# Performance work log

Measured on AMD Instinct MI355X. Metric: run time of the kernel, lower is better.

The kernel has to match this reference:

```python
import jax, jax.numpy as jnp
import numpy as np

N_NODES = 50000
N_EDGES = 1600000
FEAT = 1536
HID = 200
NCLS = 2


def setup_inputs() -> dict:
    key = jax.random.key(0)
    ks = jax.random.split(key, 12)
    x = jax.random.normal(ks[0], (N_NODES, FEAT), dtype=jnp.float32)
    edge_src = jax.random.randint(ks[1], (N_EDGES,), 0, N_NODES, dtype=jnp.int32)
    edge_dst = jax.random.randint(ks[2], (N_EDGES,), 0, N_NODES, dtype=jnp.int32)
    edge_w = jax.random.uniform(ks[3], (N_EDGES,), dtype=jnp.float32)
    s1 = 1.0 / np.sqrt(768.0)
    s2 = 1.0 / np.sqrt(HID)
    return {
        "x": x,
        "edge_src": edge_src,
        "edge_dst": edge_dst,
        "edge_w": edge_w,
        "W1a": jax.random.normal(ks[4], (768, HID), dtype=jnp.float32) * s1,
        "b1a": jnp.zeros((HID,), jnp.float32),
        "W2a": jax.random.normal(ks[5], (HID, NCLS), dtype=jnp.float32) * s2,
        "b2a": jnp.zeros((NCLS,), jnp.float32),
        "W1b": jax.random.normal(ks[6], (768, HID), dtype=jnp.float32) * s1,
        "b1b": jnp.zeros((HID,), jnp.float32),
        "W2b": jax.random.normal(ks[7], (HID, NCLS), dtype=jnp.float32) * s2,
        "b2b": jnp.zeros((NCLS,), jnp.float32),
    }


def _gcn_conv(x, W, b, src, dst, w, activation):
    # GCNConv: activation(A @ (X @ W) + b) with sparse A given as edge list
    h = x @ W                                  # [N, out] dense transform first (out < in)
    msg = h[src] * w[:, None]                  # [E, out] weighted messages
    agg = jax.ops.segment_sum(msg, dst, num_segments=x.shape[0])  # [N, out]
    return activation(agg + b)


def reference(x, edge_src, edge_dst, edge_w, W1a, b1a, W2a, b2a, W1b, b1b, W2b, b2b):
    x1 = x[:, :768]
    x2 = x[:, 768:]
    # Expert 1 branch (dropout is identity at inference)
    h1 = _gcn_conv(x1, W1a, b1a, edge_src, edge_dst, edge_w, jax.nn.relu)
    p1 = _gcn_conv(h1, W2a, b2a, edge_src, edge_dst, edge_w,
                   lambda z: jax.nn.softmax(z, axis=-1))
    # Expert 2 branch
    h2 = _gcn_conv(x2, W1b, b1b, edge_src, edge_dst, edge_w, jax.nn.relu)
    p2 = _gcn_conv(h2, W2b, b2b, edge_src, edge_dst, edge_w,
                   lambda z: jax.nn.softmax(z, axis=-1))
    # Inference-mode soft voting: elementwise max then renormalize
    votes = jnp.maximum(p1, p2)
    votes = votes / jnp.sum(votes, axis=1, keepdims=True)
    return votes
```

## Files before the change

### kernel.cpp

```cpp
#include <hip/hip_runtime.h>
#include <hip/hip_fp16.h>

#define N_NODES 50000
#define N_EDGES 1600000
#define FEAT    1536
#define HID     200
#define HIDP    208
#define HID2    416
#define KDIM    768
#define NSTRIPE 16
#define STRW    3200
#define NKEYS   (N_NODES * NSTRIPE)
#define L0B     3125
#define L1B     13

typedef _Float16 half8 __attribute__((ext_vector_type(8)));
typedef _Float16 half4 __attribute__((ext_vector_type(4)));
typedef float   float4v __attribute__((ext_vector_type(4)));

__global__ void prep_kernel(const float* __restrict__ W1a, const float* __restrict__ b1a,
                            const float* __restrict__ W2a,
                            const float* __restrict__ W1b, const float* __restrict__ b1b,
                            const float* __restrict__ W2b,
                            _Float16* __restrict__ Wht, float* __restrict__ b1comb,
                            float* __restrict__ W2comb) {
  int i = blockIdx.x * 256 + threadIdx.x;
  if (i < 2 * HIDP * KDIM) {
    int br = i / (HIDP * KDIM);
    int r  = i % (HIDP * KDIM);
    int n = r / KDIM, k = r % KDIM;
    const float* W = br ? W1b : W1a;
    Wht[i] = (n < HID) ? (_Float16)W[k * HID + n] : (_Float16)0.0f;
  }
  if (i < HID2) {
    int br = i / HIDP, c = i % HIDP;
    const float* b  = br ? b1b : b1a;
    const float* W2 = br ? W2b : W2a;
    bool ok = (c < HID);
    b1comb[i]       = ok ? b[c]        : 0.0f;
    W2comb[2*i + 0] = ok ? W2[c*2 + 0] : 0.0f;
    W2comb[2*i + 1] = ok ? W2[c*2 + 1] : 0.0f;
  }
}

__global__ void hist_kernel(const int* __restrict__ src, const int* __restrict__ dst,
                            int* __restrict__ cnt) {
  int i = blockIdx.x * 256 + threadIdx.x;
  if (i < N_EDGES) {
    int key = dst[i] * NSTRIPE + src[i] / STRW;
    atomicAdd(&cnt[key], 1);
  }
}

__global__ void scanA_kernel(const int* __restrict__ cnt, int* __restrict__ bsum) {
  __shared__ int s[256];
  int t = threadIdx.x;
  s[t] = cnt[blockIdx.x * 256 + t];
  __syncthreads();
  for (int off = 128; off; off >>= 1) {
    if (t < off) s[t] += s[t + off];
    __syncthreads();
  }
  if (t == 0) bsum[blockIdx.x] = s[0];
}
__global__ void scanM1_kernel(const int* __restrict__ bsum, int* __restrict__ bsumB) {
  __shared__ int s[256];
  int t = threadIdx.x, i = blockIdx.x * 256 + t;
  s[t] = (i < L0B) ? bsum[i] : 0;
  __syncthreads();
  for (int off = 128; off; off >>= 1) {
    if (t < off) s[t] += s[t + off];
    __syncthreads();
  }
  if (t == 0) bsumB[blockIdx.x] = s[0];
}
__global__ void scanTop_kernel(const int* __restrict__ bsumB, int* __restrict__ boff2,
                               int* __restrict__ bptr) {
  if (threadIdx.x == 0) {
    int run = 0;
    for (int j = 0; j < L1B; ++j) { boff2[j] = run; run += bsumB[j]; }
    bptr[NKEYS] = run;
  }
}
__global__ void scanMid_kernel(const int* __restrict__ bsum, const int* __restrict__ boff2,
                               int* __restrict__ boff1) {
  __shared__ int s[256];
  int t = threadIdx.x, i = blockIdx.x * 256 + t;
  int v = (i < L0B) ? bsum[i] : 0;
  s[t] = v;
  __syncthreads();
  for (int off = 1; off < 256; off <<= 1) {
    int a = (t >= off) ? s[t - off] : 0;
    __syncthreads();
    s[t] += a;
    __syncthreads();
  }
  if (i < L0B) boff1[i] = boff2[blockIdx.x] + s[t] - v;
}
__global__ void scanLow_kernel(const int* __restrict__ cnt, const int* __restrict__ boff1,
                               int* __restrict__ bptr) {
  __shared__ int s[256];
  int t = threadIdx.x, i = blockIdx.x * 256 + t;
  int v = cnt[i];
  s[t] = v;
  __syncthreads();
  for (int off = 1; off < 256; off <<= 1) {
    int a = (t >= off) ? s[t - off] : 0;
    __syncthreads();
    s[t] += a;
    __syncthreads();
  }
  bptr[i] = boff1[blockIdx.x] + s[t] - v;
}

__global__ void permute_kernel(const int* __restrict__ src, const int* __restrict__ dst,
                               const float* __restrict__ w, const int* __restrict__ bptr,
                               int* __restrict__ cnt2, int2* __restrict__ ssw) {
  int i = blockIdx.x * 256 + threadIdx.x;
  if (i < N_EDGES) {
    int key = dst[i] * NSTRIPE + src[i] / STRW;
    int pos = bptr[key] + atomicAdd(&cnt2[key], 1);
    ssw[pos] = make_int2(src[i], __float_as_int(w[i]));
  }
}

__global__ __launch_bounds__(256, 2) void gemm1_kernel(const float* __restrict__ x,
    const _Float16* __restrict__ Wht, _Float16* __restrict__ hpre) {
  const int m0 = blockIdx.x * 128;
  const int br = blockIdx.y;
  const int tid = threadIdx.x;
  const int wave = tid >> 6, lane = tid & 63;
  __shared__ _Float16 Alds[128][40];
  __shared__ _Float16 Blds[HIDP][40];
  const _Float16* Wb = Wht + (size_t)br * HIDP * KDIM;
  float4v acc[2][13];
#pragma unroll
  for (int mt = 0; mt < 2; ++mt)
#pragma unroll
    for (int nt = 0; nt < 13; ++nt) acc[mt][nt] = (float4v){0.f, 0.f, 0.f, 0.f};

  const int mlo = lane & 15, kq = (lane >> 4) * 8;

  for (int k0 = 0; k0 < KDIM; k0 += 32) {
    __syncthreads();
#pragma unroll
    for (int p = 0; p < 4; ++p) {
      int idx = tid + p * 256;
      int row = idx >> 3, c4 = idx & 7;
      int grow = m0 + row; if (grow > N_NODES - 1) grow = N_NODES - 1;
      const float4v xv = *(const float4v*)(x + (size_t)grow * FEAT + br * KDIM + k0 + c4 * 4);
      half4 hv = {(_Float16)xv[0], (_Float16)xv[1], (_Float16)xv[2], (_Float16)xv[3]};
      *(half4*)&Alds[row][c4 * 4] = hv;
    }
    for (int idx = tid; idx < HIDP * 4; idx += 256) {
      int n = idx >> 2, c = idx & 3;
      *(half8*)&Blds[n][c * 8] = *(const half8*)(Wb + n * KDIM + k0 + c * 8);
    }
    __syncthreads();
    half8 a0 = *(half8*)&Alds[wave * 32 + mlo][kq];
    half8 a1 = *(half8*)&Alds[wave * 32 + 16 + mlo][kq];
#pragma unroll
    for (int nt = 0; nt < 13; ++nt) {
      half8 b = *(half8*)&Blds[nt * 16 + mlo][kq];
      acc[0][nt] = __builtin_amdgcn_mfma_f32_16x16x32_f16(a0, b, acc[0][nt], 0, 0, 0);
      acc[1][nt] = __builtin_amdgcn_mfma_f32_16x16x32_f16(a1, b, acc[1][nt], 0, 0, 0);
    }
  }
  const int nlo = lane & 15, mq = (lane >> 4) * 4;
#pragma unroll
  for (int mt = 0; mt < 2; ++mt)
#pragma unroll
    for (int nt = 0; nt < 13; ++nt)
#pragma unroll
      for (int r = 0; r < 4; ++r) {
        int row = m0 + wave * 32 + mt * 16 + mq + r;
        if (row < N_NODES)
          hpre[(size_t)row * HID2 + br * HIDP + nt * 16 + nlo] = (_Float16)acc[mt][nt][r];
      }
}

__global__ __launch_bounds__(64) void agg1_kernel(const int2* __restrict__ ssw,
    const int* __restrict__ bptr, const _Float16* __restrict__ hpre,
    const float* __restrict__ b1comb, const float* __restrict__ W2comb,
    float4v* __restrict__ qtab) {
  const int d = blockIdx.x;
  const int lane = threadIdx.x;
  const int e0 = bptr[d * NSTRIPE], e1 = bptr[d * NSTRIPE + NSTRIPE];
  float acc[8];
#pragma unroll
  for (int j = 0; j < 8; ++j) acc[j] = 0.f;
  if (lane < 52) {
    const _Float16* hp = hpre + lane * 8;
    int e = e0;
    for (; e + 3 < e1; e += 4) {
      int2 s0 = ssw[e], s1 = ssw[e + 1], s2 = ssw[e + 2], s3 = ssw[e + 3];
      half8 h0 = *(const half8*)(hp + (size_t)s0.x * HID2);
      half8 h1 = *(const half8*)(hp + (size_t)s1.x * HID2);
      half8 h2 = *(const half8*)(hp + (size_t)s2.x * HID2);
      half8 h3 = *(const half8*)(hp + (size_t)s3.x * HID2);
      float w0 = __int_as_float(s0.y), w1 = __int_as_float(s1.y);
      float w2 = __int_as_float(s2.y), w3 = __int_as_float(s3.y);
#pragma unroll
      for (int j = 0; j < 8; ++j)
        acc[j] += w0 * (float)h0[j] + w1 * (float)h1[j]
                + w2 * (float)h2[j] + w3 * (float)h3[j];
    }
    for (; e < e1; ++e) {
      int2 s0 = ssw[e];
      half8 h0 = *(const half8*)(hp + (size_t)s0.x * HID2);
      float w0 = __int_as_float(s0.y);
#pragma unroll
      for (int j = 0; j < 8; ++j) acc[j] += w0 * (float)h0[j];
    }
  }
  float p0 = 0.f, p1 = 0.f;
  if (lane < 52) {
#pragma unroll
    for (int j = 0; j < 8; ++j) {
      int col = lane * 8 + j;
      float h = fmaxf(acc[j] + b1comb[col], 0.f);
      p0 += h * W2comb[2 * col + 0];
      p1 += h * W2comb[2 * col + 1];
    }
  }
  __shared__ float red0[64], red1[64];
  red0[lane] = p0; red1[lane] = p1;
  __syncthreads();
  if (lane == 0) {
    float q10 = 0, q11 = 0, q20 = 0, q21 = 0;
    for (int l = 0; l < 26; ++l)  { q10 += red0[l]; q11 += red1[l]; }
    for (int l = 26; l < 52; ++l) { q20 += red0[l]; q21 += red1[l]; }
    qtab[d] = (float4v){q10, q11, q20, q21};
  }
}

__global__ __launch_bounds__(256) void agg2_kernel(const int2* __restrict__ ssw,
    const int* __restrict__ bptr, const float4v* __restrict__ qtab,
    const float* __restrict__ b2a, const float* __restrict__ b2b,
    float* __restrict__ out) {
  const int d = blockIdx.x * 4 + (threadIdx.x >> 6);
  const int lane = threadIdx.x & 63;
  const int e0 = bptr[d * NSTRIPE], e1 = bptr[d * NSTRIPE + NSTRIPE];
  float a0 = 0.f, a1 = 0.f, a2 = 0.f, a3 = 0.f;
  for (int e = e0 + lane; e < e1; e += 64) {
    int2 sw = ssw[e];
    float w = __int_as_float(sw.y);
    float4v q = qtab[sw.x];
    a0 += w * q[0]; a1 += w * q[1]; a2 += w * q[2]; a3 += w * q[3];
  }
#pragma unroll
  for (int off = 32; off > 0; off >>= 1) {
    a0 += __shfl_xor(a0, off);
    a1 += __shfl_xor(a1, off);
    a2 += __shfl_xor(a2, off);
    a3 += __shfl_xor(a3, off);
  }
  if (lane == 0) {
    float za0 = a0 + b2a[0], za1 = a1 + b2a[1];
    float zb0 = a2 + b2b[0], zb1 = a3 + b2b[1];
    float m1 = fmaxf(za0, za1);
    float ea0 = __expf(za0 - m1), ea1 = __expf(za1 - m1);
    float p10 = ea0 / (ea0 + ea1), p11 = ea1 / (ea0 + ea1);
    float m2 = fmaxf(zb0, zb1);
    float eb0 = __expf(zb0 - m2), eb1 = __expf(zb1 - m2);
    float p20 = eb0 / (eb0 + eb1), p21 = eb1 / (eb0 + eb1);
    float v0 = fmaxf(p10, p20), v1 = fmaxf(p11, p21);
    float s = v0 + v1;
    out[d * 2 + 0] = v0 / s;
    out[d * 2 + 1] = v1 / s;
  }
}

extern "C" void kernel_launch(void* const* d_in, const int* in_sizes, int n_in,
                              void* d_out, int out_size, void* d_ws, size_t ws_size,
                              hipStream_t stream) {
  const float* x        = (const float*)d_in[0];
  const int*   edge_src = (const int*)d_in[1];
  const int*   edge_dst = (const int*)d_in[2];
  const float* edge_w   = (const float*)d_in[3];
  const float* W1a = (const float*)d_in[4];
  const float* b1a = (const float*)d_in[5];
  const float* W2a = (const float*)d_in[6];
  const float* b2a = (const float*)d_in[7];
  const float* W1b = (const float*)d_in[8];
  const float* b1b = (const float*)d_in[9];
  const float* W2b = (const float*)d_in[10];
  const float* b2b = (const float*)d_in[11];
  float* out = (float*)d_out;

  char* ws = (char*)d_ws;
  size_t off = 0;
  auto alloc = [&](size_t bytes) -> void* {
    void* p = ws + off;
    off = (off + bytes + 255) & ~(size_t)255;
    return p;
  };
  _Float16* Wht  = (_Float16*)alloc((size_t)2 * HIDP * KDIM * sizeof(_Float16));
  float* b1comb  = (float*)alloc(HID2 * sizeof(float));
  float* W2comb  = (float*)alloc(HID2 * 2 * sizeof(float));
  int* bptr      = (int*)alloc((NKEYS + 1) * sizeof(int));
  int* cnt       = (int*)alloc(NKEYS * sizeof(int));
  int* cnt2      = (int*)alloc(NKEYS * sizeof(int));
  int* bsum      = (int*)alloc(L0B * sizeof(int));
  int* bsumB     = (int*)alloc(L1B * sizeof(int));
  int* boff2     = (int*)alloc(L1B * sizeof(int));
  int* boff1     = (int*)alloc(L0B * sizeof(int));
  int2* ssw      = (int2*)alloc((size_t)N_EDGES * sizeof(int2));
  float4v* qtab  = (float4v*)alloc((size_t)N_NODES * sizeof(float4v));
  _Float16* hpre = (_Float16*)alloc((size_t)N_NODES * HID2 * sizeof(_Float16));
  (void)ws_size; (void)in_sizes; (void)n_in; (void)out_size;

  (void)hipMemsetAsync(cnt,  0, NKEYS * sizeof(int), stream);
  (void)hipMemsetAsync(cnt2, 0, NKEYS * sizeof(int), stream);

  prep_kernel<<<dim3((2 * HIDP * KDIM + 255) / 256), dim3(256), 0, stream>>>(
      W1a, b1a, W2a, W1b, b1b, W2b, Wht, b1comb, W2comb);
  hist_kernel<<<dim3((N_EDGES + 255) / 256), dim3(256), 0, stream>>>(edge_src, edge_dst, cnt);
  scanA_kernel<<<dim3(L0B), dim3(256), 0, stream>>>(cnt, bsum);
  scanM1_kernel<<<dim3(L1B), dim3(256), 0, stream>>>(bsum, bsumB);
  scanTop_kernel<<<dim3(1), dim3(64), 0, stream>>>(bsumB, boff2, bptr);
  scanMid_kernel<<<dim3(L1B), dim3(256), 0, stream>>>(bsum, boff2, boff1);
  scanLow_kernel<<<dim3(L0B), dim3(256), 0, stream>>>(cnt, boff1, bptr);
  permute_kernel<<<dim3((N_EDGES + 255) / 256), dim3(256), 0, stream>>>(
      edge_src, edge_dst, edge_w, bptr, cnt2, ssw);
  gemm1_kernel<<<dim3((N_NODES + 127) / 128, 2), dim3(256), 0, stream>>>(x, Wht, hpre);
  agg1_kernel<<<dim3(N_NODES), dim3(64), 0, stream>>>(ssw, bptr, hpre, b1comb, W2comb, qtab);
  agg2_kernel<<<dim3(N_NODES / 4), dim3(256), 0, stream>>>(ssw, bptr, qtab, b2a, b2b, out);
}
```

Before: 858.1 us.

## Merge scan kernels, reuse count buffer, and pack more nodes per aggregation block

```diff
diff --git a/kernel.cpp b/kernel.cpp
--- a/kernel.cpp
+++ b/kernel.cpp
@@ -63,29 +63,21 @@
   }
   if (t == 0) bsum[blockIdx.x] = s[0];
 }
-__global__ void scanM1_kernel(const int* __restrict__ bsum, int* __restrict__ bsumB) {
+
+__global__ void scanMid2_kernel(const int* __restrict__ bsum, int* __restrict__ boff1) {
   __shared__ int s[256];
-  int t = threadIdx.x, i = blockIdx.x * 256 + t;
-  s[t] = (i < L0B) ? bsum[i] : 0;
+  __shared__ int base_s;
+  int t = threadIdx.x, b = blockIdx.x, i = b * 256 + t;
+  int partial = 0;
+  for (int j = t; j < b * 256; j += 256) partial += bsum[j];
+  s[t] = partial;
   __syncthreads();
   for (int off = 128; off; off >>= 1) {
     if (t < off) s[t] += s[t + off];
     __syncthreads();
   }
-  if (t == 0) bsumB[blockIdx.x] = s[0];
-}
-__global__ void scanTop_kernel(const int* __restrict__ bsumB, int* __restrict__ boff2,
-                               int* __restrict__ bptr) {
-  if (threadIdx.x == 0) {
-    int run = 0;
-    for (int j = 0; j < L1B; ++j) { boff2[j] = run; run += bsumB[j]; }
-    bptr[NKEYS] = run;
-  }
-}
-__global__ void scanMid_kernel(const int* __restrict__ bsum, const int* __restrict__ boff2,
-                               int* __restrict__ boff1) {
-  __shared__ int s[256];
-  int t = threadIdx.x, i = blockIdx.x * 256 + t;
+  if (t == 0) base_s = s[0];
+  __syncthreads();
   int v = (i < L0B) ? bsum[i] : 0;
   s[t] = v;
   __syncthreads();
@@ -95,13 +87,15 @@
     s[t] += a;
     __syncthreads();
   }
-  if (i < L0B) boff1[i] = boff2[blockIdx.x] + s[t] - v;
-}
-__global__ void scanLow_kernel(const int* __restrict__ cnt, const int* __restrict__ boff1,
+  if (i < L0B) boff1[i] = base_s + s[t] - v;
+}
+
+__global__ void scanLow_kernel(int* __restrict__ cnt, const int* __restrict__ boff1,
                                int* __restrict__ bptr) {
   __shared__ int s[256];
   int t = threadIdx.x, i = blockIdx.x * 256 + t;
   int v = cnt[i];
+  cnt[i] = 0;
   s[t] = v;
   __syncthreads();
   for (int off = 1; off < 256; off <<= 1) {
@@ -111,15 +105,16 @@
     __syncthreads();
   }
   bptr[i] = boff1[blockIdx.x] + s[t] - v;
+  if (i == 0) bptr[NKEYS] = N_EDGES;
 }
 
 __global__ void permute_kernel(const int* __restrict__ src, const int* __restrict__ dst,
                                const float* __restrict__ w, const int* __restrict__ bptr,
-                               int* __restrict__ cnt2, int2* __restrict__ ssw) {
+                               int* __restrict__ cnt, int2* __restrict__ ssw) {
   int i = blockIdx.x * 256 + threadIdx.x;
   if (i < N_EDGES) {
     int key = dst[i] * NSTRIPE + src[i] / STRW;
-    int pos = bptr[key] + atomicAdd(&cnt2[key], 1);
+    int pos = bptr[key] + atomicAdd(&cnt[key], 1);
     ssw[pos] = make_int2(src[i], __float_as_int(w[i]));
   }
 }
@@ -179,18 +174,22 @@
       }
 }
 
-__global__ __launch_bounds__(64) void agg1_kernel(const int2* __restrict__ ssw,
+__global__ __launch_bounds__(256) void agg1_kernel(const int2* __restrict__ ssw,
     const int* __restrict__ bptr, const _Float16* __restrict__ hpre,
     const float* __restrict__ b1comb, const float* __restrict__ W2comb,
     float4v* __restrict__ qtab) {
-  const int d = blockIdx.x;
-  const int lane = threadIdx.x;
+  const int d = blockIdx.x * 4 + (threadIdx.x >> 6);
+  const int lane = threadIdx.x & 63;
+  const bool actA = (lane < 26);
+  const bool actB = (lane >= 32 && lane < 58);
+  const bool act  = actA || actB;
+  const int col = actA ? lane * 8 : (actB ? 208 + (lane - 32) * 8 : 0);
   const int e0 = bptr[d * NSTRIPE], e1 = bptr[d * NSTRIPE + NSTRIPE];
   float acc[8];
 #pragma unroll
   for (int j = 0; j < 8; ++j) acc[j] = 0.f;
-  if (lane < 52) {
-    const _Float16* hp = hpre + lane * 8;
+  if (act) {
+    const _Float16* hp = hpre + col;
     int e = e0;
     for (; e + 3 < e1; e += 4) {
       int2 s0 = ssw[e], s1 = ssw[e + 1], s2 = ssw[e + 2], s3 = ssw[e + 3];
@@ -214,42 +213,41 @@
     }
   }
   float p0 = 0.f, p1 = 0.f;
-  if (lane < 52) {
+  if (act) {
 #pragma unroll
     for (int j = 0; j < 8; ++j) {
-      int col = lane * 8 + j;
-      float h = fmaxf(acc[j] + b1comb[col], 0.f);
-      p0 += h * W2comb[2 * col + 0];
-      p1 += h * W2comb[2 * col + 1];
-    }
-  }
-  __shared__ float red0[64], red1[64];
-  red0[lane] = p0; red1[lane] = p1;
-  __syncthreads();
-  if (lane == 0) {
-    float q10 = 0, q11 = 0, q20 = 0, q21 = 0;
-    for (int l = 0; l < 26; ++l)  { q10 += red0[l]; q11 += red1[l]; }
-    for (int l = 26; l < 52; ++l) { q20 += red0[l]; q21 += red1[l]; }
-    qtab[d] = (float4v){q10, q11, q20, q21};
-  }
+      int c = col + j;
+      float h = fmaxf(acc[j] + b1comb[c], 0.f);
+      p0 += h * W2comb[2 * c + 0];
+      p1 += h * W2comb[2 * c + 1];
+    }
+  }
+#pragma unroll
+  for (int off = 16; off > 0; off >>= 1) {
+    p0 += __shfl_xor(p0, off);
+    p1 += __shfl_xor(p1, off);
+  }
+  float q2 = __shfl(p0, 32);
+  float q3 = __shfl(p1, 32);
+  if (lane == 0) qtab[d] = (float4v){p0, p1, q2, q3};
 }
 
 __global__ __launch_bounds__(256) void agg2_kernel(const int2* __restrict__ ssw,
     const int* __restrict__ bptr, const float4v* __restrict__ qtab,
     const float* __restrict__ b2a, const float* __restrict__ b2b,
     float* __restrict__ out) {
-  const int d = blockIdx.x * 4 + (threadIdx.x >> 6);
-  const int lane = threadIdx.x & 63;
+  const int d = blockIdx.x * 8 + (threadIdx.x >> 5);
+  const int lane = threadIdx.x & 31;
   const int e0 = bptr[d * NSTRIPE], e1 = bptr[d * NSTRIPE + NSTRIPE];
   float a0 = 0.f, a1 = 0.f, a2 = 0.f, a3 = 0.f;
-  for (int e = e0 + lane; e < e1; e += 64) {
+  for (int e = e0 + lane; e < e1; e += 32) {
     int2 sw = ssw[e];
     float w = __int_as_float(sw.y);
     float4v q = qtab[sw.x];
     a0 += w * q[0]; a1 += w * q[1]; a2 += w * q[2]; a3 += w * q[3];
   }
 #pragma unroll
-  for (int off = 32; off > 0; off >>= 1) {
+  for (int off = 16; off > 0; off >>= 1) {
     a0 += __shfl_xor(a0, off);
     a1 += __shfl_xor(a1, off);
     a2 += __shfl_xor(a2, off);
@@ -300,30 +298,24 @@
   float* W2comb  = (float*)alloc(HID2 * 2 * sizeof(float));
   int* bptr      = (int*)alloc((NKEYS + 1) * sizeof(int));
   int* cnt       = (int*)alloc(NKEYS * sizeof(int));
-  int* cnt2      = (int*)alloc(NKEYS * sizeof(int));
   int* bsum      = (int*)alloc(L0B * sizeof(int));
-  int* bsumB     = (int*)alloc(L1B * sizeof(int));
-  int* boff2     = (int*)alloc(L1B * sizeof(int));
   int* boff1     = (int*)alloc(L0B * sizeof(int));
   int2* ssw      = (int2*)alloc((size_t)N_EDGES * sizeof(int2));
   float4v* qtab  = (float4v*)alloc((size_t)N_NODES * sizeof(float4v));
   _Float16* hpre = (_Float16*)alloc((size_t)N_NODES * HID2 * sizeof(_Float16));
   (void)ws_size; (void)in_sizes; (void)n_in; (void)out_size;
 
-  (void)hipMemsetAsync(cnt,  0, NKEYS * sizeof(int), stream);
-  (void)hipMemsetAsync(cnt2, 0, NKEYS * sizeof(int), stream);
+  (void)hipMemsetAsync(cnt, 0, NKEYS * sizeof(int), stream);
 
   prep_kernel<<<dim3((2 * HIDP * KDIM + 255) / 256), dim3(256), 0, stream>>>(
       W1a, b1a, W2a, W1b, b1b, W2b, Wht, b1comb, W2comb);
   hist_kernel<<<dim3((N_EDGES + 255) / 256), dim3(256), 0, stream>>>(edge_src, edge_dst, cnt);
   scanA_kernel<<<dim3(L0B), dim3(256), 0, stream>>>(cnt, bsum);
-  scanM1_kernel<<<dim3(L1B), dim3(256), 0, stream>>>(bsum, bsumB);
-  scanTop_kernel<<<dim3(1), dim3(64), 0, stream>>>(bsumB, boff2, bptr);
-  scanMid_kernel<<<dim3(L1B), dim3(256), 0, stream>>>(bsum, boff2, boff1);
+  scanMid2_kernel<<<dim3(L1B), dim3(256), 0, stream>>>(bsum, boff1);
   scanLow_kernel<<<dim3(L0B), dim3(256), 0, stream>>>(cnt, boff1, bptr);
   permute_kernel<<<dim3((N_EDGES + 255) / 256), dim3(256), 0, stream>>>(
-      edge_src, edge_dst, edge_w, bptr, cnt2, ssw);
+      edge_src, edge_dst, edge_w, bptr, cnt, ssw);
   gemm1_kernel<<<dim3((N_NODES + 127) / 128, 2), dim3(256), 0, stream>>>(x, Wht, hpre);
-  agg1_kernel<<<dim3(N_NODES), dim3(64), 0, stream>>>(ssw, bptr, hpre, b1comb, W2comb, qtab);
-  agg2_kernel<<<dim3(N_NODES / 4), dim3(256), 0, stream>>>(ssw, bptr, qtab, b2a, b2b, out);
-}
+  agg1_kernel<<<dim3(N_NODES / 4), dim3(256), 0, stream>>>(ssw, bptr, hpre, b1comb, W2comb, qtab);
+  agg2_kernel<<<dim3(N_NODES / 8), dim3(256), 0, stream>>>(ssw, bptr, qtab, b2a, b2b, out);
+}
```

After: 850.0 us. About the same (-0.9%).
